# Optimization experiments

Hardware: AMD Instinct MI355X
Metric: run time of the kernel (lower is better)

The kernel has to match this reference:

```python
import jax, jax.numpy as jnp
import numpy as np
from jax import lax

B, L, C = 8, 2048, 512
H = 8
D = C // H  # head_dim = 64
FF = 4 * C


def layer_norm(x, g, b, eps=1e-5):
    mu = jnp.mean(x, axis=-1, keepdims=True)
    var = jnp.mean((x - mu) ** 2, axis=-1, keepdims=True)
    return (x - mu) * lax.rsqrt(var + eps) * g + b


def conv1d(x, w, b, groups=1):
    # x: [N, Cin, L], w: [Cout, Cin//groups, K], 'same' padding for K=3
    y = lax.conv_general_dilated(
        x, w, window_strides=(1,), padding=[(1, 1)],
        dimension_numbers=('NCH', 'OIH', 'NCH'), feature_group_count=groups)
    return y + b[None, :, None]


def setup_inputs() -> dict:
    key = jax.random.key(0)
    ks = jax.random.split(key, 12)
    s = 0.02
    inp = {
        'x': jax.random.normal(ks[0], (B, L, C), dtype=jnp.float32),
        # norm1
        'g1': jnp.ones((C,), jnp.float32), 'b1': jnp.zeros((C,), jnp.float32),
        # attention projections (stored as [in, out] for x @ W)
        'qk_w': jax.random.normal(ks[1], (C, 2 * C), jnp.float32) * s,
        'qk_b': jnp.zeros((2 * C,), jnp.float32),
        'v_w': jax.random.normal(ks[2], (C, C), jnp.float32) * s,
        'v_b': jnp.zeros((C,), jnp.float32),
        # depthwise LePE conv: [D, 1, 3], groups=D
        'lepe_w': jax.random.normal(ks[3], (D, 1, 3), jnp.float32) * s,
        'lepe_b': jnp.zeros((D,), jnp.float32),
        # norm2
        'g2': jnp.ones((C,), jnp.float32), 'b2': jnp.zeros((C,), jnp.float32),
        # GatedConv1D: inner LayerNorm + Conv1d(C, 2C, 3, pad=1); proj_out=Identity (expansion=1)
        'spn_g': jnp.ones((C,), jnp.float32), 'spn_b': jnp.zeros((C,), jnp.float32),
        'sp_cw': jax.random.normal(ks[4], (2 * C, C, 3), jnp.float32) * s,
        'sp_cb': jnp.zeros((2 * C,), jnp.float32),
        # norm3
        'g3': jnp.ones((C,), jnp.float32), 'b3': jnp.zeros((C,), jnp.float32),
        # FFN
        'w1': jax.random.normal(ks[5], (C, FF), jnp.float32) * s,
        'bb1': jnp.zeros((FF,), jnp.float32),
        'w2': jax.random.normal(ks[6], (FF, C), jnp.float32) * s,
        'bb2': jnp.zeros((C,), jnp.float32),
    }
    return inp


def _attn(x, qk_w, qk_b, v_w, v_b, lepe_w, lepe_b):
    # x: [B, L, C]
    qk = (x @ qk_w + qk_b).reshape(B, L, 2, H, D).transpose(2, 0, 3, 1, 4)
    q, k = qk[0], qk[1]                      # [B, H, L, D]
    v = (x @ v_w + v_b).reshape(B, L, H, D).transpose(0, 2, 1, 3)  # [B, H, L, D]
    q = jax.nn.elu(q) + 1.0
    k = jax.nn.elu(k) + 1.0

    def lepe(t):
        # Faithful to torch: raw row-major reshape [B,H,L,D] -> [B*H, D, L]
        # (NOT a transpose), depthwise conv along last axis, reshape back.
        c = conv1d(t.reshape(B * H, D, L), lepe_w, lepe_b, groups=D)
        return t + c.reshape(B, H, D, L).transpose(0, 1, 3, 2)

    q = lepe(q)
    k = lepe(k)
    k_mean = jnp.mean(k, axis=2, keepdims=True)                    # [B, H, 1, D]
    z = 1.0 / (jnp.einsum('bhld,bhmd->bhlm', q, k_mean) + 1e-6)    # [B, H, L, 1]
    kv = jnp.einsum('bhld,bhle->bhde', k, v) / L                   # [B, H, D, D]
    out = jnp.einsum('bhld,bhde->bhle', q, kv) * z                 # [B, H, L, D]
    return out.transpose(0, 2, 1, 3).reshape(B, L, C)


def reference(x, g1, b1, qk_w, qk_b, v_w, v_b, lepe_w, lepe_b,
              g2, b2, spn_g, spn_b, sp_cw, sp_cb, g3, b3, w1, bb1, w2, bb2):
    # Dropout is identity (eval mode).
    # Block 1: linear attention with LePE
    x = x + _attn(layer_norm(x, g1, b1), qk_w, qk_b, v_w, v_b, lepe_w, lepe_b)

    # Block 2: gated conv state path. state_path(input) = input + gated(conv(LN(input)))
    sp_in = layer_norm(x, g2, b2)
    h = layer_norm(sp_in, spn_g, spn_b)
    c = conv1d(h.transpose(0, 2, 1), sp_cw, sp_cb).transpose(0, 2, 1)  # [B, L, 2C]
    vv, gg = jnp.split(c, 2, axis=-1)
    x = x + (sp_in + vv * jax.nn.sigmoid(gg))

    # Block 3: FFN with exact GELU (torch default)
    h = layer_norm(x, g3, b3)
    x = x + (jax.nn.gelu(h @ w1 + bb1, approximate=False) @ w2 + bb2)
    return x
```

## Files before the change

kernel.cpp:

```cpp
#include <hip/hip_runtime.h>
#include <hip/hip_bf16.h>
#include <math.h>

#define Bb 8
#define Ll 2048
#define Ccn 512
#define Hh 8
#define Dd 64
#define NR (Bb * Ll)
#define PROW 2050

typedef __hip_bfloat16 bf16;
typedef __attribute__((ext_vector_type(8))) __bf16 bf16x8;
typedef __attribute__((ext_vector_type(4))) float f32x4;

#define GLDS(g, l) __builtin_amdgcn_global_load_lds(                          \
    (const __attribute__((address_space(1))) void*)(g),                       \
    (__attribute__((address_space(3))) void*)(l), 16, 0, 0)

__device__ __forceinline__ void unpack2(unsigned u, float& a, float& b) {
  union { float f; unsigned x; } lo, hi;
  lo.x = u << 16; hi.x = u & 0xffff0000u;
  a = lo.f; b = hi.f;
}

__device__ __forceinline__ float ldin(const void* p, int i, int isbf) {
  return isbf ? (float)((const bf16*)p)[i] : ((const float*)p)[i];
}

__device__ __forceinline__ void ldin8(const void* p, size_t base, int isbf, float* v) {
  if (isbf) {
    int4 q = *(const int4*)((const bf16*)p + base);
    unpack2((unsigned)q.x, v[0], v[1]); unpack2((unsigned)q.y, v[2], v[3]);
    unpack2((unsigned)q.z, v[4], v[5]); unpack2((unsigned)q.w, v[6], v[7]);
  } else {
    float4 a = *(const float4*)((const float*)p + base);
    float4 b = *(const float4*)((const float*)p + base + 4);
    v[0]=a.x; v[1]=a.y; v[2]=a.z; v[3]=a.w;
    v[4]=b.x; v[5]=b.y; v[6]=b.z; v[7]=b.w;
  }
}

__device__ __forceinline__ void st8(bf16* dst, const float* v) {
  bf16x8 o;
#pragma unroll
  for (int t = 0; t < 8; ++t) o[t] = (__bf16)v[t];
  *(bf16x8*)dst = o;
}

__global__ void detect_kernel(const unsigned* __restrict__ g1, int* __restrict__ flag) {
  *flag = ((g1[0] & 0xFFFFu) == 0x3F80u) ? 1 : 0;
}

__global__ void ln1_kernel(const void* __restrict__ x, const void* __restrict__ g,
                           const void* __restrict__ b, const int* __restrict__ dflag,
                           bf16* __restrict__ outb, float* __restrict__ xf)
{
  int isbf = *dflag;
  int row  = blockIdx.x * 4 + (threadIdx.x >> 6);
  int lane = threadIdx.x & 63;
  size_t obase = (size_t)row * Ccn + lane * 8;
  float vals[8];
  ldin8(x, obase, isbf, vals);
  float4 c0 = {vals[0], vals[1], vals[2], vals[3]};
  float4 c1 = {vals[4], vals[5], vals[6], vals[7]};
  *(float4*)(xf + obase)     = c0;
  *(float4*)(xf + obase + 4) = c1;
  float s = 0.f, q = 0.f;
#pragma unroll
  for (int a = 0; a < 8; ++a) { s += vals[a]; q += vals[a] * vals[a]; }
#pragma unroll
  for (int off = 1; off < 64; off <<= 1) {
    s += __shfl_xor(s, off);
    q += __shfl_xor(q, off);
  }
  float mu  = s * (1.f / Ccn);
  float var = q * (1.f / Ccn) - mu * mu;
  float rs  = rsqrtf(var + 1e-5f);
  float gv[8], bv[8], o[8];
  ldin8(g, lane * 8, isbf, gv);
  ldin8(b, lane * 8, isbf, bv);
#pragma unroll
  for (int a = 0; a < 8; ++a) o[a] = (vals[a] - mu) * rs * gv[a] + bv[a];
  st8(&outb[obase], o);
}

__global__ void ln_kernel(const float* __restrict__ xin, const void* __restrict__ g,
                          const void* __restrict__ b, const int* __restrict__ dflag,
                          bf16* __restrict__ outb)
{
  int isbf = *dflag;
  int row  = blockIdx.x * 4 + (threadIdx.x >> 6);
  int lane = threadIdx.x & 63;
  const float* xr = xin + (size_t)row * Ccn;
  float4 v0 = *(const float4*)(xr + lane * 8);
  float4 v1 = *(const float4*)(xr + lane * 8 + 4);
  float vals[8] = {v0.x, v0.y, v0.z, v0.w, v1.x, v1.y, v1.z, v1.w};
  float s = 0.f, q = 0.f;
#pragma unroll
  for (int a = 0; a < 8; ++a) { s += vals[a]; q += vals[a] * vals[a]; }
#pragma unroll
  for (int off = 1; off < 64; off <<= 1) {
    s += __shfl_xor(s, off);
    q += __shfl_xor(q, off);
  }
  float mu  = s * (1.f / Ccn);
  float var = q * (1.f / Ccn) - mu * mu;
  float rs  = rsqrtf(var + 1e-5f);
  size_t obase = (size_t)row * Ccn + lane * 8;
  float gv[8], bv[8], o[8];
  ldin8(g, lane * 8, isbf, gv);
  ldin8(b, lane * 8, isbf, bv);
#pragma unroll
  for (int a = 0; a < 8; ++a) o[a] = (vals[a] - mu) * rs * gv[a] + bv[a];
  st8(&outb[obase], o);
}

__global__ void glng_kernel(float* __restrict__ xf, const bf16* __restrict__ spin,
                            const bf16* __restrict__ c, const void* __restrict__ g,
                            const void* __restrict__ b, const int* __restrict__ dflag,
                            bf16* __restrict__ outb)
{
  int isbf = *dflag;
  int row  = blockIdx.x * 4 + (threadIdx.x >> 6);
  int lane = threadIdx.x & 63;
  size_t obase = (size_t)row * Ccn + lane * 8;
  int cc = lane * 8;
  float vv[8], gg[8], sp[8], xv[8];
  ldin8(&c[(size_t)row * 1024 + cc], 0, 1, vv);
  ldin8(&c[(size_t)row * 1024 + 512 + cc], 0, 1, gg);
  ldin8(&spin[obase], 0, 1, sp);
  float4 a0 = *(const float4*)&xf[obase];
  float4 a1 = *(const float4*)&xf[obase + 4];
  xv[0]=a0.x; xv[1]=a0.y; xv[2]=a0.z; xv[3]=a0.w;
  xv[4]=a1.x; xv[5]=a1.y; xv[6]=a1.z; xv[7]=a1.w;
#pragma unroll
  for (int a = 0; a < 8; ++a) xv[a] += sp[a] + vv[a] / (1.f + __expf(-gg[a]));
  float4 o0 = {xv[0], xv[1], xv[2], xv[3]};
  float4 o1 = {xv[4], xv[5], xv[6], xv[7]};
  *(float4*)&xf[obase]     = o0;
  *(float4*)&xf[obase + 4] = o1;
  float s = 0.f, q = 0.f;
#pragma unroll
  for (int a = 0; a < 8; ++a) { s += xv[a]; q += xv[a] * xv[a]; }
#pragma unroll
  for (int off = 1; off < 64; off <<= 1) {
    s += __shfl_xor(s, off);
    q += __shfl_xor(q, off);
  }
  float mu  = s * (1.f / Ccn);
  float var = q * (1.f / Ccn) - mu * mu;
  float rs  = rsqrtf(var + 1e-5f);
  float gv[8], bv[8], o[8];
  ldin8(g, lane * 8, isbf, gv);
  ldin8(b, lane * 8, isbf, bv);
#pragma unroll
  for (int a = 0; a < 8; ++a) o[a] = (xv[a] - mu) * rs * gv[a] + bv[a];
  st8(&outb[obase], o);
}

__global__ void ln2_kernel(const float* __restrict__ xin, const void* __restrict__ g,
                           const void* __restrict__ b, const void* __restrict__ sg,
                           const void* __restrict__ sb, const int* __restrict__ dflag,
                           bf16* __restrict__ sp_out, bf16* __restrict__ h_out)
{
  int isbf = *dflag;
  int row  = blockIdx.x * 4 + (threadIdx.x >> 6);
  int lane = threadIdx.x & 63;
  const float* xr = xin + (size_t)row * Ccn;
  float4 v0 = *(const float4*)(xr + lane * 8);
  float4 v1 = *(const float4*)(xr + lane * 8 + 4);
  float vals[8] = {v0.x, v0.y, v0.z, v0.w, v1.x, v1.y, v1.z, v1.w};
  float s = 0.f, q = 0.f;
#pragma unroll
  for (int a = 0; a < 8; ++a) { s += vals[a]; q += vals[a] * vals[a]; }
#pragma unroll
  for (int off = 1; off < 64; off <<= 1) {
    s += __shfl_xor(s, off);
    q += __shfl_xor(q, off);
  }
  float mu  = s * (1.f / Ccn);
  float var = q * (1.f / Ccn) - mu * mu;
  float rs  = rsqrtf(var + 1e-5f);
  size_t obase = (size_t)row * Ccn + lane * 8;
  float gv[8], bv[8], o[8];
  ldin8(g, lane * 8, isbf, gv);
  ldin8(b, lane * 8, isbf, bv);
  float s2 = 0.f, q2 = 0.f;
#pragma unroll
  for (int a = 0; a < 8; ++a) {
    o[a] = (vals[a] - mu) * rs * gv[a] + bv[a];
    s2 += o[a]; q2 += o[a] * o[a];
  }
  st8(&sp_out[obase], o);
#pragma unroll
  for (int off = 1; off < 64; off <<= 1) {
    s2 += __shfl_xor(s2, off);
    q2 += __shfl_xor(q2, off);
  }
  float mu2  = s2 * (1.f / Ccn);
  float var2 = q2 * (1.f / Ccn) - mu2 * mu2;
  float rs2  = rsqrtf(var2 + 1e-5f);
  float sgv[8], sbv[8], o2[8];
  ldin8(sg, lane * 8, isbf, sgv);
  ldin8(sb, lane * 8, isbf, sbv);
#pragma unroll
  for (int a = 0; a < 8; ++a) o2[a] = (o[a] - mu2) * rs2 * sgv[a] + sbv[a];
  size_t prow = (size_t)(row >> 11) * PROW + 1 + (row & 2047);
  st8(&h_out[prow * Ccn + lane * 8], o2);
}

__global__ void guard_zero(bf16* __restrict__ P) {
  int b = blockIdx.x;
  int t = threadIdx.x;
  size_t r0 = (size_t)b * PROW * Ccn;
  size_t r1 = r0 + (size_t)(PROW - 1) * Ccn;
  ((int*)(P + r0))[t] = 0;
  ((int*)(P + r1))[t] = 0;
}

__global__ void transpose_w(const void* __restrict__ src, bf16* __restrict__ dst,
                            const int* __restrict__ dflag, int R, int C) {
  int isbf = *dflag;
  __shared__ bf16 tile[32][33];
  int c0 = blockIdx.x * 32, r0 = blockIdx.y * 32;
  int tx = threadIdx.x & 31, ty = threadIdx.x >> 5;
#pragma unroll
  for (int i = 0; i < 32; i += 8)
    tile[ty + i][tx] = (bf16)ldin(src, (r0 + ty + i) * C + c0 + tx, isbf);
  __syncthreads();
#pragma unroll
  for (int i = 0; i < 32; i += 8)
    dst[(size_t)(c0 + ty + i) * R + r0 + tx] = tile[tx][ty + i];
}

__global__ void convw_permute(const void* __restrict__ src, bf16* __restrict__ dst,
                              const int* __restrict__ dflag) {
  int isbf = *dflag;
  int idx = blockIdx.x * 256 + threadIdx.x;
  int o = idx / 1536, j = idx - o * 1536;
  int k = j >> 9, i = j & 511;
  dst[idx] = (bf16)ldin(src, o * 1536 + i * 3 + k, isbf);
}

#define EPI_NONE  0
#define EPI_ELU1  1
#define EPI_GELU  2
#define EPI_RESID 3
#define EPI_QKV   4

template<int EPI, bool CONV>
__global__ void gemm_bt(const bf16* __restrict__ A, const bf16* __restrict__ Bt,
                        const void* __restrict__ bias, const void* __restrict__ bias2,
                        const float* __restrict__ resid,
                        void* __restrict__ out, void* __restrict__ out2,
                        const int* __restrict__ dflag,
                        int M, int Nn, int K, int orow0)
{
  int isbf = *dflag;
  __shared__ __align__(16) bf16 As[128 * 64];
  __shared__ __align__(16) bf16 Bs[128 * 64];
  int tid  = threadIdx.x;
  int wave = tid >> 6, lane = tid & 63;
  int wm = (wave >> 1) * 64, wn = (wave & 1) * 64;
  int row0 = blockIdx.x * 128;
  int col0 = blockIdx.y * 128;
  f32x4 acc[4][4] = {};
  int m_in = lane & 15;
  int kq   = lane >> 4;
  int r8   = lane >> 3;
  int swz8 = (((lane & 7) - r8) & 7) * 8;
  size_t prow0 = 0;
  if (CONV) {
    int bb = row0 >> 11, l0 = row0 & 2047;
    prow0 = (size_t)bb * PROW + l0;
  }

  for (int k0 = 0; k0 < K; k0 += 64) {
    {
      int cw = col0 + wave * 32;
#pragma unroll
      for (int g = 0; g < 4; ++g)
        GLDS(&Bt[(size_t)(cw + g*8 + r8) * K + k0 + swz8], &Bs[(wave*32 + g*8) * 64]);
    }
    if (CONV) {
      int kpos = k0 >> 9;
      int ii   = (k0 & 511) + swz8;
#pragma unroll
      for (int g = 0; g < 4; ++g) {
        size_t rs = prow0 + wave*32 + g*8 + r8 + kpos;
        GLDS(&A[rs * 512 + ii], &As[(wave*32 + g*8) * 64]);
      }
    } else {
#pragma unroll
      for (int g = 0; g < 4; ++g)
        GLDS(&A[(size_t)(row0 + wave*32 + g*8 + r8) * K + k0 + swz8],
             &As[(wave*32 + g*8) * 64]);
    }
    __syncthreads();
#pragma unroll
    for (int kk = 0; kk < 2; ++kk) {
      int Cu = kk * 4 + kq;
      bf16x8 af[4], bfr[4];
#pragma unroll
      for (int i = 0; i < 4; ++i) {
        int R = wm + i * 16 + m_in;
        af[i] = *(const bf16x8*)&As[R * 64 + ((Cu + R) & 7) * 8];
      }
#pragma unroll
      for (int j = 0; j < 4; ++j) {
        int R = wn + j * 16 + m_in;
        bfr[j] = *(const bf16x8*)&Bs[R * 64 + ((Cu + R) & 7) * 8];
      }
#pragma unroll
      for (int i = 0; i < 4; ++i)
#pragma unroll
        for (int j = 0; j < 4; ++j)
          acc[i][j] = __builtin_amdgcn_mfma_f32_16x16x32_bf16(af[i], bfr[j], acc[i][j], 0, 0, 0);
    }
    __syncthreads();
  }

  const int ESTR = 72;
  bf16* eb = As + wave * (16 * ESTR);
  int col_in = lane & 15;
  int row_in = (lane >> 4) * 4;
  int rr = lane >> 3;
  int cb = (lane & 7) * 8;
#pragma unroll
  for (int i = 0; i < 4; ++i) {
#pragma unroll
    for (int j = 0; j < 4; ++j) {
      int col = col0 + wn + j * 16 + col_in;
      float bv = (EPI == EPI_QKV)
          ? ((col < 1024) ? ldin(bias, col, isbf) : ldin(bias2, col - 1024, isbf))
          : ldin(bias, col, isbf);
#pragma unroll
      for (int r = 0; r < 4; ++r) {
        float v = acc[i][j][r] + bv;
        if (EPI == EPI_ELU1) v = (v > 0.f) ? (v + 1.f) : __expf(v);
        if (EPI == EPI_QKV && col < 1024) v = (v > 0.f) ? (v + 1.f) : __expf(v);
        if (EPI == EPI_GELU) {
          float u = v * (0.7978845608f + 0.0356774081f * v * v);
          u = fminf(fmaxf(u, -10.f), 10.f);
          float e = __expf(2.f * u);
          v = v * e / (e + 1.f);
        }
        eb[(row_in + r) * ESTR + j * 16 + col_in] = (bf16)v;
      }
    }
    int row = row0 + wm + i * 16;
#pragma unroll
    for (int s = 0; s < 2; ++s) {
      int r2 = rr + s * 8;
      bf16x8 pk = *(const bf16x8*)&eb[r2 * ESTR + cb];
      int grow = row + r2;
      int col  = col0 + wn + cb;
      if (EPI == EPI_RESID) {
        size_t gbase = (size_t)(grow + orow0) * Nn + col;
        float4 ra = *(const float4*)&resid[gbase];
        float4 rb = *(const float4*)&resid[gbase + 4];
        float vv[8];
#pragma unroll
        for (int t = 0; t < 8; ++t) vv[t] = (float)pk[t];
        vv[0]+=ra.x; vv[1]+=ra.y; vv[2]+=ra.z; vv[3]+=ra.w;
        vv[4]+=rb.x; vv[5]+=rb.y; vv[6]+=rb.z; vv[7]+=rb.w;
        if (isbf) {
          st8(&((bf16*)out)[gbase], vv);
        } else {
          float4 o0 = {vv[0], vv[1], vv[2], vv[3]};
          float4 o1 = {vv[4], vv[5], vv[6], vv[7]};
          *(float4*)&((float*)out)[gbase]     = o0;
          *(float4*)&((float*)out)[gbase + 4] = o1;
        }
      } else if (EPI == EPI_QKV) {
        if (col < 1024)
          *(bf16x8*)&((bf16*)out)[(size_t)grow * 1024 + col] = pk;
        else
          *(bf16x8*)&((bf16*)out2)[(size_t)grow * 512 + (col - 1024)] = pk;
      } else {
        *(bf16x8*)&((bf16*)out)[(size_t)grow * Nn + col] = pk;
      }
    }
  }
}

template<int SRCOFF, int DSTSTR, bool DOKM>
__global__ void lepe2_kernel(const bf16* __restrict__ qk, bf16* __restrict__ dst,
                             const void* __restrict__ w, const void* __restrict__ cb,
                             const int* __restrict__ dflag, float* __restrict__ km) {
  int isbf = *dflag;
  __shared__ float buf[64][66];
  int bh = blockIdx.y; int b = bh >> 3, h = bh & 7;
  int tile = blockIdx.x;
  int t = threadIdx.x;
  int r  = t >> 3;
  int o8 = (t & 7) * 8;
  size_t sbase = (size_t)b * 2048 * 1024 + SRCOFF + h * 64;

  int4 cv[2], id[2];
#pragma unroll
  for (int it = 0; it < 2; ++it) {
    int ch = r + it * 32;
    cv[it] = *(const int4*)&qk[sbase + (size_t)(ch * 32 + tile) * 1024 + o8];
    id[it] = *(const int4*)&qk[sbase + (size_t)(tile * 64 + ch) * 1024 + o8];
  }
  float edge = 0.f; int eidx = -1, espot = 0;
  if (t < 64) {
    eidx = t; espot = 0;
    if (tile > 0) edge = (float)qk[sbase + (size_t)(t * 32 + tile - 1) * 1024 + 63];
  } else if (t < 128) {
    eidx = t - 64; espot = 65;
    if (tile < 31) edge = (float)qk[sbase + (size_t)((t - 64) * 32 + tile + 1) * 1024 + 0];
  }
  float w0[2], w1[2], w2[2], bi[2];
#pragma unroll
  for (int it = 0; it < 2; ++it) {
    int ch = r + it * 32;
    w0[it] = ldin(w, ch * 3 + 0, isbf);
    w1[it] = ldin(w, ch * 3 + 1, isbf);
    w2[it] = ldin(w, ch * 3 + 2, isbf);
    bi[it] = ldin(cb, ch, isbf);
  }
#pragma unroll
  for (int it = 0; it < 2; ++it) {
    float v[8];
    unpack2((unsigned)cv[it].x, v[0], v[1]); unpack2((unsigned)cv[it].y, v[2], v[3]);
    unpack2((unsigned)cv[it].z, v[4], v[5]); unpack2((unsigned)cv[it].w, v[6], v[7]);
    int ch = r + it * 32;
#pragma unroll
    for (int k = 0; k < 8; ++k) buf[ch][1 + o8 + k] = v[k];
  }
  if (eidx >= 0) buf[eidx][espot] = edge;
  __syncthreads();
  float co[2][8];
#pragma unroll
  for (int it = 0; it < 2; ++it) {
    int ch = r + it * 32;
    float a0 = buf[ch][o8], a1 = buf[ch][o8 + 1];
#pragma unroll
    for (int k = 0; k < 8; ++k) {
      float a2 = buf[ch][o8 + 2 + k];
      co[it][k] = bi[it] + w0[it] * a0 + w1[it] * a1 + w2[it] * a2;
      a0 = a1; a1 = a2;
    }
  }
  __syncthreads();
#pragma unroll
  for (int it = 0; it < 2; ++it) {
    int ch = r + it * 32;
#pragma unroll
    for (int k = 0; k < 8; ++k) buf[o8 + k][ch] = co[it][k];
  }
  __syncthreads();
  float psum[8];
#pragma unroll
  for (int k = 0; k < 8; ++k) psum[k] = 0.f;
#pragma unroll
  for (int it = 0; it < 2; ++it) {
    int lr = r + it * 32;
    float v[8];
    unpack2((unsigned)id[it].x, v[0], v[1]); unpack2((unsigned)id[it].y, v[2], v[3]);
    unpack2((unsigned)id[it].z, v[4], v[5]); unpack2((unsigned)id[it].w, v[6], v[7]);
#pragma unroll
    for (int k = 0; k < 8; ++k) {
      v[k] += buf[lr][o8 + k];
      if (DOKM) psum[k] += v[k];
    }
    st8(&dst[(size_t)(b * 2048 + tile * 64 + lr) * DSTSTR + h * 64 + o8], v);
  }
  if (DOKM) {
    __syncthreads();
#pragma unroll
    for (int k = 0; k < 8; ++k) buf[r][o8 + k] = psum[k];
    __syncthreads();
    if (t < 64) {
      float s = 0.f;
#pragma unroll 8
      for (int rr2 = 0; rr2 < 32; ++rr2) s += buf[rr2][t];
      atomicAdd(&km[bh * 64 + t], s * (1.f / 2048.f));
    }
  }
}

__global__ void kv_kernel(const bf16* __restrict__ k2, const bf16* __restrict__ v,
                          float* __restrict__ kv) {
  int bh = blockIdx.x, split = blockIdx.y;
  int b = bh >> 3, h = bh & 7;
  int t = threadIdx.x;
  __shared__ __align__(16) bf16 ks[64][64];
  __shared__ __align__(16) bf16 vs[64][64];
  int d0 = (t & 15) * 4, e0 = (t >> 4) * 4;
  int lr = t >> 2, q4 = (t & 3) * 16;
  float acc[4][4] = {};
  for (int chunk = 0; chunk < 4; ++chunk) {
    int l = split * 256 + chunk * 64 + lr;
    size_t rk = ((size_t)(b*2048 + l)) * 1024 + h*64 + q4;
    size_t rv = ((size_t)(b*2048 + l)) * 512 + h*64 + q4;
    *(int4*)&ks[lr][q4]     = *(const int4*)&k2[rk];
    *(int4*)&ks[lr][q4 + 8] = *(const int4*)&k2[rk + 8];
    *(int4*)&vs[lr][q4]     = *(const int4*)&v[rv];
    *(int4*)&vs[lr][q4 + 8] = *(const int4*)&v[rv + 8];
    __syncthreads();
    for (int l2 = 0; l2 < 64; ++l2) {
      float kvv[4], vvv[4];
#pragma unroll
      for (int a = 0; a < 4; ++a) kvv[a] = (float)ks[l2][d0 + a];
#pragma unroll
      for (int a = 0; a < 4; ++a) vvv[a] = (float)vs[l2][e0 + a];
#pragma unroll
      for (int a = 0; a < 4; ++a)
#pragma unroll
        for (int c = 0; c < 4; ++c) acc[a][c] += kvv[a] * vvv[c];
    }
    __syncthreads();
  }
  const float sc = 1.f / 2048.f;
#pragma unroll
  for (int a = 0; a < 4; ++a)
#pragma unroll
    for (int c = 0; c < 4; ++c)
      atomicAdd(&kv[(size_t)(bh*64 + d0 + a) * 64 + e0 + c], acc[a][c] * sc);
}

__global__ void attn_out_kernel(const bf16* __restrict__ q2, const float* __restrict__ kv,
                                const float* __restrict__ kmean, float* __restrict__ xf) {
  int bh = blockIdx.x; int b = bh >> 3, h = bh & 7;
  int lbase = blockIdx.y * 64;
  int t = threadIdx.x;
  __shared__ float kvs[64][65];
  __shared__ float km[64];
  for (int i = t; i < 64*64; i += 256) kvs[i >> 6][i & 63] = kv[(size_t)bh*4096 + i];
  if (t < 64) km[t] = kmean[bh*64 + t];
  __syncthreads();
  int lr = t >> 2, eg = (t & 3) * 16;
  int l = lbase + lr;
  size_t qrow = ((size_t)(b*2048 + l)) * 512 + h*64;
  float qv[64];
#pragma unroll
  for (int d8 = 0; d8 < 64; d8 += 8) {
    int4 p = *(const int4*)&q2[qrow + d8];
    unpack2((unsigned)p.x, qv[d8+0], qv[d8+1]);
    unpack2((unsigned)p.y, qv[d8+2], qv[d8+3]);
    unpack2((unsigned)p.z, qv[d8+4], qv[d8+5]);
    unpack2((unsigned)p.w, qv[d8+6], qv[d8+7]);
  }
  float zd = 0.f;
#pragma unroll
  for (int d = 0; d < 64; ++d) zd += qv[d] * km[d];
  float z = 1.f / (zd + 1e-6f);
  float sacc[16] = {};
#pragma unroll
  for (int d = 0; d < 64; ++d) {
    float qd = qv[d];
    const float* row = &kvs[d][eg];
#pragma unroll
    for (int i = 0; i < 16; ++i) sacc[i] += qd * row[i];
  }
  size_t xrow = ((size_t)(b*2048 + l)) * 512 + h*64 + eg;
#pragma unroll
  for (int s = 0; s < 4; ++s) {
    float4 cur = *(const float4*)&xf[xrow + s * 4];
    cur.x += sacc[s*4+0] * z; cur.y += sacc[s*4+1] * z;
    cur.z += sacc[s*4+2] * z; cur.w += sacc[s*4+3] * z;
    *(float4*)&xf[xrow + s * 4] = cur;
  }
}

__global__ void gating_kernel(float* __restrict__ xf, const bf16* __restrict__ spin,
                              const bf16* __restrict__ c) {
  size_t idx = ((size_t)blockIdx.x * 256 + threadIdx.x) * 8;
  size_t n = idx >> 9; int cc = (int)(idx & 511);
  float vv[8], gg[8], sp[8];
  ldin8(&c[n * 1024 + cc], 0, 1, vv);
  ldin8(&c[n * 1024 + 512 + cc], 0, 1, gg);
  ldin8(&spin[idx], 0, 1, sp);
#pragma unroll
  for (int s = 0; s < 2; ++s) {
    float4 cur = *(const float4*)&xf[idx + s * 4];
    float* cp = &cur.x;
#pragma unroll
    for (int t = 0; t < 4; ++t) {
      int a = s * 4 + t;
      cp[t] += sp[a] + vv[a] / (1.f + __expf(-gg[a]));
    }
    *(float4*)&xf[idx + s * 4] = cur;
  }
}

extern "C" void kernel_launch(void* const* d_in, const int* in_sizes, int n_in,
                              void* d_out, int out_size, void* d_ws, size_t ws_size,
                              hipStream_t stream) {
  (void)in_sizes; (void)n_in; (void)out_size;
  const void* x      = d_in[0];
  const void* g1     = d_in[1];
  const void* b1     = d_in[2];
  const void* qk_w   = d_in[3];
  const void* qk_b   = d_in[4];
  const void* v_w    = d_in[5];
  const void* v_b    = d_in[6];
  const void* lepe_w = d_in[7];
  const void* lepe_b = d_in[8];
  const void* g2     = d_in[9];
  const void* b2     = d_in[10];
  const void* spn_g  = d_in[11];
  const void* spn_b  = d_in[12];
  const void* sp_cw  = d_in[13];
  const void* sp_cb  = d_in[14];
  const void* g3     = d_in[15];
  const void* b3     = d_in[16];
  const void* w1     = d_in[17];
  const void* bb1    = d_in[18];
  const void* w2     = d_in[19];
  const void* bb2    = d_in[20];

  char* ws = (char*)d_ws;
  const size_t MB = 1 << 20;
  const bool big = ws_size >= (size_t)129 * MB;

  bf16*  qk_wT  = (bf16*)(ws);
  bf16*  v_wT   = (bf16*)(ws + 0x100000);
  bf16*  convWT = (bf16*)(ws + 0x180000);
  bf16*  w1T    = (bf16*)(ws + 0x480000);
  bf16*  w2T    = (bf16*)(ws + 0x680000);
  float* kmean  = (float*)(ws + 0x880000);
  float* kvb    = (float*)(ws + 0x890000);
  int*   dflag  = (int*)(ws + 0x990000);
  float* xf     = (float*)(ws + 16*MB);
  bf16*  ybf    = (bf16*)(ws + 48*MB);
  bf16*  qkbuf  = (bf16*)(ws + 64*MB);
  bf16*  spbuf  = ybf;
  bf16*  ybf2p  = (bf16*)(ws + 64*MB);
  bf16*  cbufS  = (bf16*)(ws + 96*MB);
  bf16*  cbufB  = (bf16*)(ws + 96*MB);
  bf16*  tbuf   = (bf16*)(ws + 64*MB);
  bf16*  vout   = (bf16*)d_out;

  detect_kernel<<<1, 1, 0, stream>>>((const unsigned*)g1, dflag);
  hipMemsetAsync(kvb, 0, 64 * 64 * 64 * sizeof(float), stream);
  hipMemsetAsync(kmean, 0, 64 * 64 * sizeof(float), stream);

  transpose_w<<<dim3(32, 16), 256, 0, stream>>>(qk_w, qk_wT, dflag, 512, 1024);
  transpose_w<<<dim3(16, 16), 256, 0, stream>>>(v_w,  v_wT,  dflag, 512, 512);
  transpose_w<<<dim3(64, 16), 256, 0, stream>>>(w1,   w1T,   dflag, 512, 2048);
  transpose_w<<<dim3(16, 64), 256, 0, stream>>>(w2,   w2T,   dflag, 2048, 512);
  convw_permute<<<1024*1536/256, 256, 0, stream>>>(sp_cw, convWT, dflag);

  ln1_kernel<<<NR/4, 256, 0, stream>>>(x, g1, b1, dflag, ybf, xf);
  gemm_bt<EPI_QKV, false><<<dim3(128, 12), 256, 0, stream>>>(
      ybf, qk_wT, qk_b, v_b, nullptr, qkbuf, vout, dflag, NR, 1536, 512, 0);
  lepe2_kernel<0,   512,  false><<<dim3(32, 64), 256, 0, stream>>>(
      qkbuf, ybf, lepe_w, lepe_b, dflag, nullptr);
  lepe2_kernel<512, 1024, true ><<<dim3(32, 64), 256, 0, stream>>>(
      qkbuf, qkbuf, lepe_w, lepe_b, dflag, kmean);
  kv_kernel<<<dim3(64, 8), 256, 0, stream>>>(qkbuf, vout, kvb);
  attn_out_kernel<<<dim3(64, 32), 256, 0, stream>>>(ybf, kvb, kmean, xf);

  guard_zero<<<8, 256, 0, stream>>>(ybf2p);
  ln2_kernel<<<NR/4, 256, 0, stream>>>(xf, g2, b2, spn_g, spn_b, dflag, spbuf, ybf2p);
  if (big) {
    gemm_bt<EPI_NONE, true><<<dim3(128, 8), 256, 0, stream>>>(
        ybf2p, convWT, sp_cb, nullptr, nullptr, cbufB, nullptr, dflag, NR, 1024, 1536, 0);
    glng_kernel<<<NR/4, 256, 0, stream>>>(xf, spbuf, cbufB, g3, b3, dflag, ybf);
  } else {
    for (int half = 0; half < 2; ++half) {
      size_t ro = (size_t)half * 8192;
      gemm_bt<EPI_NONE, true><<<dim3(64, 8), 256, 0, stream>>>(
          ybf2p + (ro >> 11) * PROW * 512, convWT, sp_cb, nullptr, nullptr,
          cbufS, nullptr, dflag, 8192, 1024, 1536, 0);
      gating_kernel<<<8192*512/2048, 256, 0, stream>>>(xf + ro*512, spbuf + ro*512, cbufS);
    }
    ln_kernel<<<NR/4, 256, 0, stream>>>(xf, g3, b3, dflag, ybf);
  }

  if (big) {
    gemm_bt<EPI_GELU,  false><<<dim3(128, 16), 256, 0, stream>>>(
        ybf, w1T, bb1, nullptr, nullptr, tbuf, nullptr, dflag, NR, 2048, 512, 0);
    gemm_bt<EPI_RESID, false><<<dim3(128, 4),  256, 0, stream>>>(
        tbuf, w2T, bb2, nullptr, xf, d_out, nullptr, dflag, NR, 512, 2048, 0);
  } else {
    for (int half = 0; half < 2; ++half) {
      size_t ro = (size_t)half * 8192;
      gemm_bt<EPI_GELU,  false><<<dim3(64, 16), 256, 0, stream>>>(
          ybf + ro*512, w1T, bb1, nullptr, nullptr, tbuf, nullptr, dflag, 8192, 2048, 512, 0);
      gemm_bt<EPI_RESID, false><<<dim3(64, 4),  256, 0, stream>>>(
          tbuf, w2T, bb2, nullptr, xf, d_out, nullptr, dflag, 8192, 512, 2048, (int)ro);
    }
  }
}
```

Before: 523.7 us.

## Use fast reciprocal, hoist epilogue bias loads, vectorize LDS reads in attention kernels

Replaces IEEE divisions in the gating, GELU epilogue and attention normalizer with the hardware approximate reciprocal. Hoists the per-column bias and ELU flag out of the row loop in the GEMM epilogue. Vectorizes LDS reads in the kv and attn_out kernels and pads the kv tile row to 68 floats so rows stay 16-byte aligned for float4 loads. These are small instruction-count micro-optimizations, and the approximate reciprocal slightly lowers precision.

```diff
diff --git a/kernel.cpp b/kernel.cpp
--- a/kernel.cpp
+++ b/kernel.cpp
@@ -23,6 +23,8 @@
   lo.x = u << 16; hi.x = u & 0xffff0000u;
   a = lo.f; b = hi.f;
 }
+
+__device__ __forceinline__ float frcp(float x) { return __builtin_amdgcn_rcpf(x); }
 
 __device__ __forceinline__ float ldin(const void* p, int i, int isbf) {
   return isbf ? (float)((const bf16*)p)[i] : ((const float*)p)[i];
@@ -135,7 +137,7 @@
   xv[0]=a0.x; xv[1]=a0.y; xv[2]=a0.z; xv[3]=a0.w;
   xv[4]=a1.x; xv[5]=a1.y; xv[6]=a1.z; xv[7]=a1.w;
 #pragma unroll
-  for (int a = 0; a < 8; ++a) xv[a] += sp[a] + vv[a] / (1.f + __expf(-gg[a]));
+  for (int a = 0; a < 8; ++a) xv[a] += sp[a] + vv[a] * frcp(1.f + __expf(-gg[a]));
   float4 o0 = {xv[0], xv[1], xv[2], xv[3]};
   float4 o1 = {xv[4], xv[5], xv[6], xv[7]};
   *(float4*)&xf[obase]     = o0;
@@ -327,24 +329,33 @@
   int row_in = (lane >> 4) * 4;
   int rr = lane >> 3;
   int cb = (lane & 7) * 8;
+  float bvj[4];
+  bool  eluj[4];
+#pragma unroll
+  for (int j = 0; j < 4; ++j) {
+    int col = col0 + wn + j * 16 + col_in;
+    if (EPI == EPI_QKV) {
+      eluj[j] = (col < 1024);
+      bvj[j] = eluj[j] ? ldin(bias, col, isbf) : ldin(bias2, col - 1024, isbf);
+    } else {
+      bvj[j] = ldin(bias, col, isbf);
+      eluj[j] = false;
+    }
+  }
 #pragma unroll
   for (int i = 0; i < 4; ++i) {
 #pragma unroll
     for (int j = 0; j < 4; ++j) {
-      int col = col0 + wn + j * 16 + col_in;
-      float bv = (EPI == EPI_QKV)
-          ? ((col < 1024) ? ldin(bias, col, isbf) : ldin(bias2, col - 1024, isbf))
-          : ldin(bias, col, isbf);
 #pragma unroll
       for (int r = 0; r < 4; ++r) {
-        float v = acc[i][j][r] + bv;
+        float v = acc[i][j][r] + bvj[j];
         if (EPI == EPI_ELU1) v = (v > 0.f) ? (v + 1.f) : __expf(v);
-        if (EPI == EPI_QKV && col < 1024) v = (v > 0.f) ? (v + 1.f) : __expf(v);
+        if (EPI == EPI_QKV && eluj[j]) v = (v > 0.f) ? (v + 1.f) : __expf(v);
         if (EPI == EPI_GELU) {
           float u = v * (0.7978845608f + 0.0356774081f * v * v);
           u = fminf(fmaxf(u, -10.f), 10.f);
           float e = __expf(2.f * u);
-          v = v * e / (e + 1.f);
+          v = v * e * frcp(e + 1.f);
         }
         eb[(row_in + r) * ESTR + j * 16 + col_in] = (bf16)v;
       }
@@ -504,10 +515,10 @@
     __syncthreads();
     for (int l2 = 0; l2 < 64; ++l2) {
       float kvv[4], vvv[4];
-#pragma unroll
-      for (int a = 0; a < 4; ++a) kvv[a] = (float)ks[l2][d0 + a];
-#pragma unroll
-      for (int a = 0; a < 4; ++a) vvv[a] = (float)vs[l2][e0 + a];
+      int2 kp = *(const int2*)&ks[l2][d0];
+      int2 vp = *(const int2*)&vs[l2][e0];
+      unpack2((unsigned)kp.x, kvv[0], kvv[1]); unpack2((unsigned)kp.y, kvv[2], kvv[3]);
+      unpack2((unsigned)vp.x, vvv[0], vvv[1]); unpack2((unsigned)vp.y, vvv[2], vvv[3]);
 #pragma unroll
       for (int a = 0; a < 4; ++a)
 #pragma unroll
@@ -528,7 +539,7 @@
   int bh = blockIdx.x; int b = bh >> 3, h = bh & 7;
   int lbase = blockIdx.y * 64;
   int t = threadIdx.x;
-  __shared__ float kvs[64][65];
+  __shared__ float kvs[64][68];
   __shared__ float km[64];
   for (int i = t; i < 64*64; i += 256) kvs[i >> 6][i & 63] = kv[(size_t)bh*4096 + i];
   if (t < 64) km[t] = kmean[bh*64 + t];
@@ -548,14 +559,17 @@
   float zd = 0.f;
 #pragma unroll
   for (int d = 0; d < 64; ++d) zd += qv[d] * km[d];
-  float z = 1.f / (zd + 1e-6f);
+  float z = frcp(zd + 1e-6f);
   float sacc[16] = {};
 #pragma unroll
   for (int d = 0; d < 64; ++d) {
     float qd = qv[d];
-    const float* row = &kvs[d][eg];
-#pragma unroll
-    for (int i = 0; i < 16; ++i) sacc[i] += qd * row[i];
+    const float4* row = (const float4*)&kvs[d][eg];
+    float4 r0 = row[0], r1 = row[1], r2 = row[2], r3 = row[3];
+    sacc[0]  += qd * r0.x; sacc[1]  += qd * r0.y; sacc[2]  += qd * r0.z; sacc[3]  += qd * r0.w;
+    sacc[4]  += qd * r1.x; sacc[5]  += qd * r1.y; sacc[6]  += qd * r1.z; sacc[7]  += qd * r1.w;
+    sacc[8]  += qd * r2.x; sacc[9]  += qd * r2.y; sacc[10] += qd * r2.z; sacc[11] += qd * r2.w;
+    sacc[12] += qd * r3.x; sacc[13] += qd * r3.y; sacc[14] += qd * r3.z; sacc[15] += qd * r3.w;
   }
   size_t xrow = ((size_t)(b*2048 + l)) * 512 + h*64 + eg;
 #pragma unroll
@@ -582,7 +596,7 @@
 #pragma unroll
     for (int t = 0; t < 4; ++t) {
       int a = s * 4 + t;
-      cp[t] += sp[a] + vv[a] / (1.f + __expf(-gg[a]));
+      cp[t] += sp[a] + vv[a] * frcp(1.f + __expf(-gg[a]));
     }
     *(float4*)&xf[idx + s * 4] = cur;
   }
```

Result: faster. 460.2 us (median of 3 runs) (-12.1%).
